# Performance work log

Hardware: AMD Instinct MI355X
Metric: run time of the kernel (lower is better)

## Reference

```python
import jax, jax.numpy as jnp
import numpy as np

NEG = -1e9

def symmetric_quantize(x, bits=8):
    qmax = 2 ** (bits - 1) - 1
    scale = jnp.max(jnp.abs(x)) / qmax
    xq = jnp.clip(jnp.round(x / scale), -(qmax + 1), qmax)
    return xq * scale

def setup_inputs() -> dict:
    key = jax.random.key(0)
    k1, k2, k3, k4, k5 = jax.random.split(key, 5)
    B, S, D = 2, 2048, 1024
    hidden_states = jax.random.normal(k1, (B, S, D), dtype=jnp.float32)
    # additive causal mask [1,1,S,S]
    causal = jnp.tril(jnp.ones((S, S), dtype=bool))
    attention_mask = jnp.where(causal, 0.0, NEG).astype(jnp.float32)[None, None]
    # weights stored (out,in) as used by F.linear; pre-quantized at init (weight_bits=8)
    W_attn = symmetric_quantize(jax.random.normal(k2, (3 * D, D), dtype=jnp.float32) * 0.02)
    b_attn = jax.random.normal(k3, (3 * D,), dtype=jnp.float32) * 0.02
    W_proj = symmetric_quantize(jax.random.normal(k4, (D, D), dtype=jnp.float32) * 0.02)
    b_proj = jax.random.normal(k5, (D,), dtype=jnp.float32) * 0.02
    return {"hidden_states": hidden_states, "attention_mask": attention_mask,
            "W_attn": W_attn, "b_attn": b_attn, "W_proj": W_proj, "b_proj": b_proj}

def reference(hidden_states, attention_mask, W_attn, b_attn, W_proj, b_proj):
    B, S, D = hidden_states.shape
    H = 16
    hd = D // H
    scale = 1.0 / jnp.sqrt(jnp.float32(hd))
    qkv = jnp.einsum('bsd,ed->bse', hidden_states, W_attn) + b_attn  # [B,S,3D]
    q, k, v = jnp.split(qkv, 3, axis=-1)
    def split_heads(x):
        return x.reshape(B, S, H, hd).transpose(0, 2, 1, 3)  # [B,H,S,hd]
    q, k, v = split_heads(q), split_heads(k), split_heads(v)
    # KV-cache fake quant (kv_bits=8)
    k = symmetric_quantize(k)
    v = symmetric_quantize(v)
    present = (k, v)
    scores = jnp.einsum('bhqd,bhkd->bhqk', q, k) * scale + attention_mask
    probs = jax.nn.softmax(scores, axis=-1)  # dropout is identity in eval
    out = jnp.einsum('bhqk,bhkd->bhqd', probs, v)
    out = out.transpose(0, 2, 1, 3).reshape(B, S, D)
    out = symmetric_quantize(out)  # activation fake quant (act_bits=8)
    out = jnp.einsum('bsd,ed->bse', out, W_proj) + b_proj
    return (out, present)
```

## Files before the change

### kernel.cpp

```cpp
#include <hip/hip_runtime.h>
#include <stdint.h>


typedef __attribute__((ext_vector_type(8))) short short8;
typedef __attribute__((ext_vector_type(4))) float floatx4;

#define SSCALE 0.18033688011112042f
#define MASKVAL -30000.0f
#define MREF 16.0f

__device__ __forceinline__ float bf2f(uint16_t s) {
  return __uint_as_float(((uint32_t)s) << 16);
}
__device__ __forceinline__ uint16_t f2bf(float f) {
  uint32_t u = __float_as_uint(f);
  u += 0x7fffu + ((u >> 16) & 1u);
  return (uint16_t)(u >> 16);
}
__device__ __forceinline__ uint64_t pack4(float a, float b, float c, float d) {
  return (uint64_t)f2bf(a) | ((uint64_t)f2bf(b) << 16) | ((uint64_t)f2bf(c) << 32) |
         ((uint64_t)f2bf(d) << 48);
}
__device__ __forceinline__ float quantize(float v, float inv, float scale) {
  return fminf(fmaxf(rintf(v * inv), -128.f), 127.f) * scale;
}
__device__ __forceinline__ void async_cp16(const void* g, void* l) {
  __builtin_amdgcn_global_load_lds((const __attribute__((address_space(1))) void*)g,
                                   (__attribute__((address_space(3))) void*)l, 16, 0, 0);
}
__device__ __forceinline__ int swz(int row, int bcol) {
  return (row * 128 + bcol) ^ ((row & 7) << 4);
}

#define WAITN(n)                                     \
  asm volatile("s_waitcnt vmcnt(" #n ")" ::: "memory"); \
  __builtin_amdgcn_s_barrier();                      \
  __builtin_amdgcn_sched_barrier(0)

__global__ void cvt_kernel(const float* __restrict__ hs, const float* __restrict__ wa,
                           const float* __restrict__ wp, uint16_t* __restrict__ hs_b,
                           uint16_t* __restrict__ wa_b, uint16_t* __restrict__ wp_b) {
  const size_t qi = (size_t)blockIdx.x * 256 + threadIdx.x;
  const float* src;
  uint16_t* dst;
  size_t off;
  if (qi < 1048576) {
    src = hs; dst = hs_b; off = qi;
  } else if (qi < 1835008) {
    src = wa; dst = wa_b; off = qi - 1048576;
  } else {
    src = wp; dst = wp_b; off = qi - 1835008;
  }
  const float4 f = ((const float4*)src)[off];
  ((uint64_t*)dst)[off] = pack4(f.x, f.y, f.z, f.w);
}

__global__ __launch_bounds__(256) void gemm_qkv(const uint16_t* __restrict__ A,
                                                const uint16_t* __restrict__ W,
                                                const float* __restrict__ bias,
                                                uint16_t* __restrict__ q_ws,
                                                float* __restrict__ kd,
                                                float* __restrict__ vd,
                                                float* __restrict__ scal) {
  __shared__ uint16_t a_sh[3][128 * 32];
  __shared__ uint16_t b_sh[3][128 * 32];
  __shared__ float wred[4];
  const int tid = threadIdx.x;
  const int lane = tid & 63, wid = tid >> 6;
  const int quad = lane >> 4, l16 = lane & 15;
  const int m0 = blockIdx.y * 128, n0 = blockIdx.x * 128;
  const int wrow = (wid >> 1) * 64, wcol = (wid & 1) * 64;
  const uint16_t* Ab = A + (size_t)m0 * 1024;
  const uint16_t* Wb = W + (size_t)n0 * 1024;

  floatx4 acc[4][4] = {};

  auto stage = [&](int buf, int k0) {
#pragma unroll
    for (int i = 0; i < 2; ++i) {
      const int chunk = tid + 256 * i;
      async_cp16(Ab + (size_t)(chunk >> 2) * 1024 + k0 + (chunk & 3) * 8,
                 (char*)a_sh[buf] + (size_t)(wid * 64 + 256 * i) * 16);
      async_cp16(Wb + (size_t)(chunk >> 2) * 1024 + k0 + (chunk & 3) * 8,
                 (char*)b_sh[buf] + (size_t)(wid * 64 + 256 * i) * 16);
    }
  };

  auto compute = [&](int cur) {
    short8 af[4], bfr[4];
#pragma unroll
    for (int mi = 0; mi < 4; ++mi)
      af[mi] = *(const short8*)&a_sh[cur][(wrow + mi * 16 + l16) * 32 + quad * 8];
#pragma unroll
    for (int ni = 0; ni < 4; ++ni)
      bfr[ni] = *(const short8*)&b_sh[cur][(wcol + ni * 16 + l16) * 32 + quad * 8];
#pragma unroll
    for (int mi = 0; mi < 4; ++mi)
#pragma unroll
      for (int ni = 0; ni < 4; ++ni)
        acc[mi][ni] =
            __builtin_amdgcn_mfma_f32_16x16x32_bf16(af[mi], bfr[ni], acc[mi][ni], 0, 0, 0);
  };

  stage(0, 0);
  stage(1, 32);
  for (int t = 0; t < 10; ++t) {
    const int k = t * 96;
    WAITN(4);
    stage(2, k + 64);
    compute(0);
    WAITN(4);
    stage(0, k + 96);
    compute(1);
    WAITN(4);
    stage(1, k + 128);
    compute(2);
  }
  WAITN(4);
  compute(0);
  WAITN(0);
  compute(1);

  const int cat = n0 >> 10;
  float tmax = 0.f;
#pragma unroll
  for (int mi = 0; mi < 4; ++mi) {
#pragma unroll
    for (int ni = 0; ni < 4; ++ni) {
      const int col = n0 + wcol + ni * 16 + l16;
      const float bv = bias[col];
#pragma unroll
      for (int r = 0; r < 4; ++r) {
        const int row = m0 + wrow + mi * 16 + quad * 4 + r;
        const float v = acc[mi][ni][r] + bv;
        if (cat == 0) {
          q_ws[(size_t)row * 1024 + col] = f2bf(v * SSCALE);
        } else {
          const int cc = col & 1023, h = cc >> 6, dd = cc & 63;
          const int b = row >> 11, s = row & 2047;
          float* dst = (cat == 1) ? kd : vd;
          dst[(((size_t)b * 16 + h) * 2048 + s) * 64 + dd] = v;
          tmax = fmaxf(tmax, fabsf(v));
        }
      }
    }
  }
  if (cat > 0) {
#pragma unroll
    for (int off = 32; off; off >>= 1) tmax = fmaxf(tmax, __shfl_xor(tmax, off));
    if (lane == 0) wred[wid] = tmax;
    __syncthreads();
    if (tid == 0) {
      const float m = fmaxf(fmaxf(wred[0], wred[1]), fmaxf(wred[2], wred[3]));
      atomicMax((unsigned int*)(scal + (cat - 1)), __float_as_uint(m));
    }
  }
}

__global__ void quant_kv(float* __restrict__ kd, float* __restrict__ vd,
                         const float* __restrict__ scal, uint16_t* __restrict__ kc,
                         uint16_t* __restrict__ vt) {
  __shared__ uint16_t tile[64 * 65];
  const int t = blockIdx.z, bh = blockIdx.y, s0 = blockIdx.x * 64;
  const float mx = t ? scal[1] : scal[0];
  const float scale = mx / 127.f;
  const float inv = (mx > 0.f) ? 127.f / mx : 0.f;
  float* base = (t ? vd : kd) + ((size_t)bh * 2048 + s0) * 64;
  const int tid = threadIdx.x;
#pragma unroll
  for (int i = 0; i < 16; ++i) {
    const int e = tid + 256 * i;
    const float q = quantize(base[e], inv, scale);
    base[e] = q;
    if (t)
      tile[(e >> 6) * 65 + (e & 63)] = f2bf(q);
    else
      kc[((size_t)bh * 2048 + s0) * 64 + e] = f2bf(q);
  }
  if (t) {
    __syncthreads();
#pragma unroll
    for (int i = 0; i < 16; ++i) {
      const int e = tid + 256 * i;
      const int dd = e >> 6, sr = e & 63;
      vt[((size_t)bh * 64 + dd) * 2048 + s0 + sr] = tile[sr * 65 + dd];
    }
  }
}

__global__ __launch_bounds__(512) void attn_kernel(const uint16_t* __restrict__ q_ws,
                                                   const uint16_t* __restrict__ kc,
                                                   const uint16_t* __restrict__ vt,
                                                   uint16_t* __restrict__ at,
                                                   float* __restrict__ omax) {
  __shared__ uint16_t qp_sh[128 * 64];
  __shared__ uint16_t k_sh[2][64 * 64];
  __shared__ uint16_t v_sh[2][64 * 64];
  __shared__ float wred[8];

  const int tid = threadIdx.x, lane = tid & 63, wid = tid >> 6;
  const int quad = lane >> 4, l16 = lane & 15;
  const int qt = (blockIdx.y & 16) ? (int)blockIdx.x : (15 - (int)blockIdx.x);
  const int bh = blockIdx.y;
  const int b = bh >> 4, h = bh & 15;
  const int wq0 = wid * 16;
  const int sr = tid >> 3, sc8 = (tid & 7) * 8;
  const uint16_t* kbase = kc + (size_t)bh * 131072;
  const uint16_t* vtbase = vt + (size_t)bh * 131072;

  const int q0 = qt * 128;
  const int jmax = 2 * qt + 1;
  const int base = q0 + wq0;
  const int rowg = base + l16;

  uint4 kr = *(const uint4*)&kbase[tid * 8];
  uint4 vr = *(const uint4*)&vtbase[(size_t)sr * 2048 + sc8];

#pragma unroll
  for (int i = 0; i < 2; ++i) {
    const int idx = tid + 512 * i;
    const int r = idx >> 3, c8 = (idx & 7) * 8;
    *(uint4*)((char*)qp_sh + swz(r, c8 * 2)) =
        *(const uint4*)&q_ws[(size_t)(b * 2048 + q0 + r) * 1024 + h * 64 + c8];
  }
  *(uint4*)((char*)k_sh[0] + swz(sr, sc8 * 2)) = kr;
  *(uint4*)((char*)v_sh[0] + swz(sr, sc8 * 2)) = vr;
  __syncthreads();

  short8 qa[2];
#pragma unroll
  for (int ks = 0; ks < 2; ++ks)
    qa[ks] = *(const short8*)((const char*)qp_sh + swz(wq0 + l16, ks * 64 + quad * 16));

  const int pr = wq0 + l16;

  floatx4 o[4] = {};
  float lst = 0.f;

  for (int j = 0; j <= jmax; ++j) {
    const int cur = j & 1;
    uint4 krn, vrn;
    if (j < jmax) {
      krn = *(const uint4*)&kbase[(size_t)(j + 1) * 4096 + tid * 8];
      vrn = *(const uint4*)&vtbase[(size_t)sr * 2048 + (j + 1) * 64 + sc8];
    }
    __builtin_amdgcn_sched_barrier(0);

    const int jb = j * 64;
    if (jb <= base + 15) {
      floatx4 s[4] = {};
#pragma unroll
      for (int ks = 0; ks < 2; ++ks) {
        short8 kf[4];
#pragma unroll
        for (int ni = 0; ni < 4; ++ni)
          kf[ni] = *(const short8*)((const char*)k_sh[cur] +
                                    swz(ni * 16 + l16, ks * 64 + quad * 16));
#pragma unroll
        for (int ni = 0; ni < 4; ++ni)
          s[ni] = __builtin_amdgcn_mfma_f32_16x16x32_bf16(kf[ni], qa[ks], s[ni], 0, 0, 0);
      }

      if (jb + 63 > base) {
#pragma unroll
        for (int ni = 0; ni < 4; ++ni)
#pragma unroll
          for (int r = 0; r < 4; ++r)
            if (jb + ni * 16 + quad * 4 + r > rowg) s[ni][r] = MASKVAL;
      }

#pragma unroll
      for (int ni = 0; ni < 4; ++ni) {
        const float e0 = exp2f(s[ni][0] - MREF);
        const float e1 = exp2f(s[ni][1] - MREF);
        const float e2 = exp2f(s[ni][2] - MREF);
        const float e3 = exp2f(s[ni][3] - MREF);
        lst += (e0 + e1) + (e2 + e3);
        uint32_t w0, w1;
        asm("v_cvt_pk_bf16_f32 %0, %1, %2" : "=v"(w0) : "v"(e0), "v"(e1));
        asm("v_cvt_pk_bf16_f32 %0, %1, %2" : "=v"(w1) : "v"(e2), "v"(e3));
        uint2 pw;
        pw.x = w0;
        pw.y = w1;
        *(uint2*)((char*)qp_sh + swz(pr, ni * 32 + quad * 8)) = pw;
      }

#pragma unroll
      for (int ks = 0; ks < 2; ++ks) {
        const short8 pb = *(const short8*)((const char*)qp_sh + swz(pr, ks * 64 + quad * 16));
        short8 vf[4];
#pragma unroll
        for (int ni = 0; ni < 4; ++ni)
          vf[ni] = *(const short8*)((const char*)v_sh[cur] +
                                    swz(ni * 16 + l16, ks * 64 + quad * 16));
#pragma unroll
        for (int ni = 0; ni < 4; ++ni)
          o[ni] = __builtin_amdgcn_mfma_f32_16x16x32_bf16(vf[ni], pb, o[ni], 0, 0, 0);
      }
    }

    if (j < jmax) {
      *(uint4*)((char*)k_sh[1 - cur] + swz(sr, sc8 * 2)) = krn;
      *(uint4*)((char*)v_sh[1 - cur] + swz(sr, sc8 * 2)) = vrn;
    }
    __syncthreads();
  }

  float l = lst;
  l += __shfl_xor(l, 16);
  l += __shfl_xor(l, 32);
  const float invl = 1.f / fmaxf(l, 1e-38f);
  const size_t rowoff = (size_t)(b * 2048 + rowg) * 1024 + h * 64;
  float tmax = 0.f;
#pragma unroll
  for (int ni = 0; ni < 4; ++ni) {
    const float v0 = o[ni][0] * invl;
    const float v1 = o[ni][1] * invl;
    const float v2 = o[ni][2] * invl;
    const float v3 = o[ni][3] * invl;
    tmax = fmaxf(tmax, fmaxf(fmaxf(fabsf(v0), fabsf(v1)), fmaxf(fabsf(v2), fabsf(v3))));
    *(uint64_t*)&at[rowoff + ni * 16 + quad * 4] = pack4(v0, v1, v2, v3);
  }

#pragma unroll
  for (int off = 32; off; off >>= 1) tmax = fmaxf(tmax, __shfl_xor(tmax, off));
  if (lane == 0) wred[wid] = tmax;
  __syncthreads();
  if (tid == 0) {
    float m = wred[0];
#pragma unroll
    for (int i = 1; i < 8; ++i) m = fmaxf(m, wred[i]);
    atomicMax((unsigned int*)omax, __float_as_uint(m));
  }
}

__global__ void quant_act(uint16_t* __restrict__ a, const float* __restrict__ omax) {
  const size_t i = ((size_t)blockIdx.x * 256 + threadIdx.x) * 8;
  const float mx = *omax;
  const float scale = mx / 127.f;
  const float inv = (mx > 0.f) ? 127.f / mx : 0.f;
  uint16_t v[8];
  *(uint4*)v = *(const uint4*)&a[i];
#pragma unroll
  for (int k = 0; k < 8; ++k) v[k] = f2bf(quantize(bf2f(v[k]), inv, scale));
  *(uint4*)&a[i] = *(const uint4*)v;
}

__global__ __launch_bounds__(256) void gemm_proj(const uint16_t* __restrict__ A,
                                                 const uint16_t* __restrict__ W,
                                                 const float* __restrict__ bias,
                                                 float* __restrict__ C) {
  __shared__ uint16_t sh[3][12288];
  const int tid = threadIdx.x;
  const int lane = tid & 63, wid = tid >> 6;
  const int quad = lane >> 4, l16 = lane & 15;
  const int m0 = blockIdx.y * 128, n0 = blockIdx.x * 64;
  const int wrow = (wid >> 1) * 64, wcol = (wid & 1) * 32;
  const uint16_t* Ab = A + (size_t)m0 * 1024;
  const uint16_t* Wb = W + (size_t)n0 * 1024;

  floatx4 acc[4][2] = {};

  auto stage = [&](int buf, int k0) {
#pragma unroll
    for (int h = 0; h < 2; ++h) {
      const int kh = k0 + h * 32;
#pragma unroll
      for (int i = 0; i < 2; ++i) {
        const int chunk = tid + 256 * i;
        async_cp16(Ab + (size_t)(chunk >> 2) * 1024 + kh + (chunk & 3) * 8,
                   (char*)&sh[buf][h * 4096] + (size_t)(wid * 64 + 256 * i) * 16);
      }
      async_cp16(Wb + (size_t)(tid >> 2) * 1024 + kh + (tid & 3) * 8,
                 (char*)&sh[buf][8192 + h * 2048] + (size_t)(wid * 64) * 16);
    }
  };

  auto compute = [&](int cur) {
    short8 af[4][2], bfr[2][2];
#pragma unroll
    for (int h = 0; h < 2; ++h) {
#pragma unroll
      for (int mi = 0; mi < 4; ++mi)
        af[mi][h] =
            *(const short8*)&sh[cur][h * 4096 + (wrow + mi * 16 + l16) * 32 + quad * 8];
#pragma unroll
      for (int ni = 0; ni < 2; ++ni)
        bfr[ni][h] = *(const short8*)&sh[cur][8192 + h * 2048 +
                                             (wcol + ni * 16 + l16) * 32 + quad * 8];
    }
#pragma unroll
    for (int mi = 0; mi < 4; ++mi)
#pragma unroll
      for (int ni = 0; ni < 2; ++ni) {
        acc[mi][ni] = __builtin_amdgcn_mfma_f32_16x16x32_bf16(af[mi][0], bfr[ni][0],
                                                              acc[mi][ni], 0, 0, 0);
        acc[mi][ni] = __builtin_amdgcn_mfma_f32_16x16x32_bf16(af[mi][1], bfr[ni][1],
                                                              acc[mi][ni], 0, 0, 0);
      }
  };

  stage(0, 0);
  stage(1, 64);
  for (int t = 0; t < 4; ++t) {
    const int k = t * 192;
    WAITN(6);
    stage(2, k + 128);
    compute(0);
    WAITN(6);
    stage(0, k + 192);
    compute(1);
    WAITN(6);
    stage(1, k + 256);
    compute(2);
  }
  WAITN(6);
  stage(2, 896);
  compute(0);
  WAITN(6);
  stage(0, 960);
  compute(1);
  WAITN(6);
  compute(2);
  WAITN(0);
  compute(0);

#pragma unroll
  for (int mi = 0; mi < 4; ++mi) {
#pragma unroll
    for (int ni = 0; ni < 2; ++ni) {
      const int col = n0 + wcol + ni * 16 + l16;
      const float bv = bias[col];
#pragma unroll
      for (int r = 0; r < 4; ++r) {
        const int row = m0 + wrow + mi * 16 + quad * 4 + r;
        C[(size_t)row * 1024 + col] = acc[mi][ni][r] + bv;
      }
    }
  }
}

extern "C" void kernel_launch(void* const* d_in, const int* in_sizes, int n_in,
                              void* d_out, int out_size, void* d_ws, size_t ws_size,
                              hipStream_t stream) {
  const float* hs = (const float*)d_in[0];
  const float* Wa = (const float*)d_in[2];
  const float* ba = (const float*)d_in[3];
  const float* Wp = (const float*)d_in[4];
  const float* bp = (const float*)d_in[5];

  float* outd = (float*)d_out;
  float* kd = outd + (size_t)4194304;
  float* vd = outd + (size_t)8388608;

  char* ws = (char*)d_ws;
  const size_t MB = 1024 * 1024;
  uint16_t* hs_b = (uint16_t*)ws;
  uint16_t* Wa_b = (uint16_t*)(ws + 8 * MB);
  uint16_t* Wp_b = (uint16_t*)(ws + 14 * MB);
  uint16_t* q_ws = (uint16_t*)(ws + 16 * MB);
  uint16_t* kc = (uint16_t*)(ws + 24 * MB);
  uint16_t* vt = (uint16_t*)(ws + 32 * MB);
  uint16_t* at = (uint16_t*)(ws + 40 * MB);
  float* scal = (float*)(ws + 48 * MB);

  hipMemsetAsync(scal, 0, 4 * sizeof(float), stream);
  cvt_kernel<<<8192, 256, 0, stream>>>(hs, Wa, Wp, hs_b, Wa_b, Wp_b);
  gemm_qkv<<<dim3(24, 32), 256, 0, stream>>>(hs_b, Wa_b, ba, q_ws, kd, vd, scal);
  quant_kv<<<dim3(32, 32, 2), 256, 0, stream>>>(kd, vd, scal, kc, vt);
  attn_kernel<<<dim3(16, 32), 512, 0, stream>>>(q_ws, kc, vt, at, scal + 2);
  quant_act<<<2048, 256, 0, stream>>>(at, scal + 2);
  gemm_proj<<<dim3(16, 32), 256, 0, stream>>>(at, Wp_b, bp, outd);
}
```

Before: 210.8 us.

## Stage 128-key K/V tiles directly into LDS with async copies

The attention kernel now loads K and V tiles straight from global memory into LDS with global_load_lds, replacing register staging. Each tile now covers 128 keys, so one barrier serves two 64-key compute chunks. V gets a 256-byte-row swizzle to fit the wider tile, and the warp-reduction scratch now reuses the Q/P buffer. This aims to cut barrier count and the register round trip for K/V, at the cost of doubled K/V LDS use (about 80KB per block) and reliance on the barrier waiting for the async copies.

Result: no change. 210.5 us (-0.2%).

```diff
diff --git a/kernel.cpp b/kernel.cpp
--- a/kernel.cpp
+++ b/kernel.cpp
@@ -30,6 +30,9 @@
 }
 __device__ __forceinline__ int swz(int row, int bcol) {
   return (row * 128 + bcol) ^ ((row & 7) << 4);
+}
+__device__ __forceinline__ int swz256(int row, int bcol) {
+  return (row * 256 + bcol) ^ ((row & 15) << 4);
 }
 
 #define WAITN(n)                                     \
@@ -194,9 +197,8 @@
                                                    uint16_t* __restrict__ at,
                                                    float* __restrict__ omax) {
   __shared__ uint16_t qp_sh[128 * 64];
-  __shared__ uint16_t k_sh[2][64 * 64];
-  __shared__ uint16_t v_sh[2][64 * 64];
-  __shared__ float wred[8];
+  __shared__ uint16_t k_sh[2][128 * 64];
+  __shared__ uint16_t v_sh[2][64 * 128];
 
   const int tid = threadIdx.x, lane = tid & 63, wid = tid >> 6;
   const int quad = lane >> 4, l16 = lane & 15;
@@ -204,17 +206,33 @@
   const int bh = blockIdx.y;
   const int b = bh >> 4, h = bh & 15;
   const int wq0 = wid * 16;
-  const int sr = tid >> 3, sc8 = (tid & 7) * 8;
-  const uint16_t* kbase = kc + (size_t)bh * 131072;
-  const uint16_t* vtbase = vt + (size_t)bh * 131072;
+  const char* kcb = (const char*)(kc + (size_t)bh * 131072);
+  const char* vtb = (const char*)(vt + (size_t)bh * 131072);
 
   const int q0 = qt * 128;
-  const int jmax = 2 * qt + 1;
+  const int nt = qt + 1;
   const int base = q0 + wq0;
   const int rowg = base + l16;
 
-  uint4 kr = *(const uint4*)&kbase[tid * 8];
-  uint4 vr = *(const uint4*)&vtbase[(size_t)sr * 2048 + sc8];
+  int ku[2], vu[2];
+#pragma unroll
+  for (int i = 0; i < 2; ++i) {
+    const int d = i * 8192 + tid * 16;
+    ku[i] = d ^ (((d >> 7) & 7) << 4);
+    const int uv = d ^ (((d >> 8) & 15) << 4);
+    vu[i] = (uv >> 8) * 4096 + (uv & 255);
+  }
+  auto stageKV = [&](int buf, int j) {
+#pragma unroll
+    for (int i = 0; i < 2; ++i) {
+      async_cp16(kcb + (size_t)j * 16384 + ku[i],
+                 (char*)k_sh[buf] + i * 8192 + wid * 1024);
+      async_cp16(vtb + (size_t)j * 256 + vu[i],
+                 (char*)v_sh[buf] + i * 8192 + wid * 1024);
+    }
+  };
+
+  stageKV(0, 0);
 
 #pragma unroll
   for (int i = 0; i < 2; ++i) {
@@ -223,8 +241,6 @@
     *(uint4*)((char*)qp_sh + swz(r, c8 * 2)) =
         *(const uint4*)&q_ws[(size_t)(b * 2048 + q0 + r) * 1024 + h * 64 + c8];
   }
-  *(uint4*)((char*)k_sh[0] + swz(sr, sc8 * 2)) = kr;
-  *(uint4*)((char*)v_sh[0] + swz(sr, sc8 * 2)) = vr;
   __syncthreads();
 
   short8 qa[2];
@@ -237,17 +253,16 @@
   floatx4 o[4] = {};
   float lst = 0.f;
 
-  for (int j = 0; j <= jmax; ++j) {
+  for (int j = 0; j < nt; ++j) {
     const int cur = j & 1;
-    uint4 krn, vrn;
-    if (j < jmax) {
-      krn = *(const uint4*)&kbase[(size_t)(j + 1) * 4096 + tid * 8];
-      vrn = *(const uint4*)&vtbase[(size_t)sr * 2048 + (j + 1) * 64 + sc8];
-    }
+    if (j + 1 < nt) stageKV(1 - cur, j + 1);
     __builtin_amdgcn_sched_barrier(0);
 
-    const int jb = j * 64;
-    if (jb <= base + 15) {
+#pragma unroll
+    for (int c = 0; c < 2; ++c) {
+      const int jb = j * 128 + c * 64;
+      if (jb > base + 15) break;
+
       floatx4 s[4] = {};
 #pragma unroll
       for (int ks = 0; ks < 2; ++ks) {
@@ -255,7 +270,7 @@
 #pragma unroll
         for (int ni = 0; ni < 4; ++ni)
           kf[ni] = *(const short8*)((const char*)k_sh[cur] +
-                                    swz(ni * 16 + l16, ks * 64 + quad * 16));
+                                    swz(c * 64 + ni * 16 + l16, ks * 64 + quad * 16));
 #pragma unroll
         for (int ni = 0; ni < 4; ++ni)
           s[ni] = __builtin_amdgcn_mfma_f32_16x16x32_bf16(kf[ni], qa[ks], s[ni], 0, 0, 0);
@@ -287,22 +302,19 @@
 
 #pragma unroll
       for (int ks = 0; ks < 2; ++ks) {
-        const short8 pb = *(const short8*)((const char*)qp_sh + swz(pr, ks * 64 + quad * 16));
+        const short8 pb =
+            *(const short8*)((const char*)qp_sh + swz(pr, ks * 64 + quad * 16));
         short8 vf[4];
 #pragma unroll
         for (int ni = 0; ni < 4; ++ni)
           vf[ni] = *(const short8*)((const char*)v_sh[cur] +
-                                    swz(ni * 16 + l16, ks * 64 + quad * 16));
+                                    swz256(ni * 16 + l16, c * 128 + ks * 64 + quad * 16));
 #pragma unroll
         for (int ni = 0; ni < 4; ++ni)
           o[ni] = __builtin_amdgcn_mfma_f32_16x16x32_bf16(vf[ni], pb, o[ni], 0, 0, 0);
       }
     }
 
-    if (j < jmax) {
-      *(uint4*)((char*)k_sh[1 - cur] + swz(sr, sc8 * 2)) = krn;
-      *(uint4*)((char*)v_sh[1 - cur] + swz(sr, sc8 * 2)) = vrn;
-    }
     __syncthreads();
   }
 
@@ -322,6 +334,7 @@
     *(uint64_t*)&at[rowoff + ni * 16 + quad * 4] = pack4(v0, v1, v2, v3);
   }
 
+  float* wred = (float*)qp_sh;
 #pragma unroll
   for (int off = 32; off; off >>= 1) tmax = fmaxf(tmax, __shfl_xor(tmax, off));
   if (lane == 0) wred[wid] = tmax;
```
